# Kernel tuning notes

Hardware: AMD Instinct MI355X
Metric: run time of the kernel (lower is better)

## Reference

```python
import jax, jax.numpy as jnp
import numpy as np

EMBED = 1024
HEADS = 16


def setup_inputs() -> dict:
    key = jax.random.key(0)
    k1, k2, k3 = jax.random.split(key, 3)
    B, S, D = 2, 2048, EMBED
    x = jax.random.normal(k1, (B, S, D), dtype=jnp.float32)
    # nn.Linear weights: stored as [out, in]; y = x @ W.T
    w_qkv = jax.random.normal(k2, (3 * D, D), dtype=jnp.float32) * (D ** -0.5)
    w_out = jax.random.normal(k3, (D, D), dtype=jnp.float32) * (D ** -0.5)
    return {"x": x, "w_qkv": w_qkv, "w_out": w_out}


def reference(x, w_qkv, w_out):
    B, S, D = x.shape
    H = HEADS
    hd = D // H
    qkv = x @ w_qkv.T                       # [B, S, 3D]
    q, k, v = jnp.split(qkv, 3, axis=-1)
    # 'b l (head k) -> b head l k'
    def heads(t):
        return t.reshape(B, S, H, hd).transpose(0, 2, 1, 3)
    q, k, v = heads(q), heads(k), heads(v)
    scale = hd ** 0.5
    scores = jnp.einsum('bhqd,bhkd->bhqk', q, k) / scale
    probs = jax.nn.softmax(scores, axis=-1)
    out = jnp.einsum('bhqk,bhkd->bhqd', probs, v)  # [B, H, S, hd]
    out = out.transpose(0, 2, 1, 3).reshape(B, S, D)
    return out @ w_out.T
```

## Files before the change

kernel.cpp:

```cpp
#include <hip/hip_runtime.h>

typedef short short8 __attribute__((ext_vector_type(8)));
typedef short short4v __attribute__((ext_vector_type(4)));
typedef float floatx4 __attribute__((ext_vector_type(4)));
typedef unsigned short ushort_t;

#define EMBED 1024
#define HEADS 16
#define HD 64
#define SEQ 2048
#define BATCH 2
#define QSCALE 0.18033688f

__device__ inline ushort_t f2bf(float f) {
    unsigned int u = __float_as_uint(f);
    u += 0x7fff + ((u >> 16) & 1);
    return (ushort_t)(u >> 16);
}

typedef const __attribute__((address_space(1))) unsigned int* gas_t;
typedef __attribute__((address_space(3))) unsigned int* las_t;
__device__ inline void async_copy16(const ushort_t* g, ushort_t* l) {
    __builtin_amdgcn_global_load_lds((gas_t)g, (las_t)l, 16, 0, 0);
}

__global__ void cast3_kernel(const float* __restrict__ a, ushort_t* __restrict__ oa, int na,
                             const float* __restrict__ b, ushort_t* __restrict__ ob, int nb,
                             const float* __restrict__ c, ushort_t* __restrict__ oc, int nc) {
    int idx = (blockIdx.x * blockDim.x + threadIdx.x) * 4;
    const float* in; ushort_t* out;
    if (idx < na)            { in = a;  out = oa; }
    else if (idx < na + nb)  { in = b;  out = ob; idx -= na; }
    else if (idx < na + nb + nc) { in = c; out = oc; idx -= na + nb; }
    else return;
    float4 f = *(const float4*)(in + idx);
    ushort4 o;
    o.x = f2bf(f.x); o.y = f2bf(f.y); o.z = f2bf(f.z); o.w = f2bf(f.w);
    *(ushort4*)(out + idx) = o;
}

#define BM 128
#define BN 128
#define BK 64

template<int MODE>
__launch_bounds__(256, 3)
__global__ void gemm_bt(const ushort_t* __restrict__ A, const ushort_t* __restrict__ B,
                        float* __restrict__ outF,
                        ushort_t* __restrict__ qb, ushort_t* __restrict__ kb,
                        ushort_t* __restrict__ vtb,
                        int M, int N, int K) {
    __shared__ ushort_t As[BM * BK];
    __shared__ ushort_t Bs[BN * BK];
    const int id   = blockIdx.x;
    const int jj   = id >> 3;
    const int bm   = (id & 7) * 4 + (jj & 3);
    const int bn   = jj >> 2;
    const int t    = threadIdx.x;
    const int lane = t & 63;
    const int wave = t >> 6;
    const int wm   = (wave >> 1) * 64;
    const int wn   = (wave & 1) * 64;
    const int m0   = bm * BM;
    const int n0   = bn * BN;
    const int col  = lane & 15;
    const int quad = lane >> 4;

    const int srow = lane >> 3;
    const int sgr  = (lane & 7) ^ (srow & 7);
    const int slot0 = quad ^ (col & 7);

    floatx4 acc[4][4] = {};

    for (int k0 = 0; k0 < K; k0 += BK) {
        for (int half = 0; half < 4; ++half) {
            int row0 = wave * 32 + half * 8;
            int r = row0 + srow;
            async_copy16(A + (size_t)(m0 + r) * K + k0 + sgr * 8, &As[row0 * BK]);
            async_copy16(B + (size_t)(n0 + r) * K + k0 + sgr * 8, &Bs[row0 * BK]);
        }
        __syncthreads();
        short8 a[2][4], b[2][4];
        for (int i = 0; i < 4; ++i) {
            int base = (wm + i * 16 + col) * BK;
            a[0][i] = *(const short8*)(&As[base + slot0 * 8]);
            a[1][i] = *(const short8*)(&As[base + (slot0 ^ 4) * 8]);
        }
        for (int j = 0; j < 4; ++j) {
            int base = (wn + j * 16 + col) * BK;
            b[0][j] = *(const short8*)(&Bs[base + slot0 * 8]);
            b[1][j] = *(const short8*)(&Bs[base + (slot0 ^ 4) * 8]);
        }
        for (int kk = 0; kk < 2; ++kk)
            for (int i = 0; i < 4; ++i)
                for (int j = 0; j < 4; ++j)
                    acc[i][j] = __builtin_amdgcn_mfma_f32_16x16x32_bf16(a[kk][i], b[kk][j], acc[i][j], 0, 0, 0);
        __syncthreads();
    }

    for (int i = 0; i < 4; ++i)
        for (int j = 0; j < 4; ++j) {
            int n = n0 + wn + j * 16 + col;
            int mb = m0 + wm + i * 16 + quad * 4;
            if (MODE == 1) {
                for (int r = 0; r < 4; ++r)
                    outF[(size_t)(mb + r) * N + n] = acc[i][j][r];
            } else {
                int part = n >> 10;
                int within = n & 1023;
                int h = within >> 6, d = within & 63;
                int bb = mb >> 11, s = mb & 2047;
                if (part == 2) {
                    short4v pv;
                    pv.x = (short)f2bf(acc[i][j][0]); pv.y = (short)f2bf(acc[i][j][1]);
                    pv.z = (short)f2bf(acc[i][j][2]); pv.w = (short)f2bf(acc[i][j][3]);
                    *(short4v*)(vtb + (((size_t)bb * HEADS + h) * HD + d) * SEQ + s) = pv;
                } else {
                    ushort_t* dst = (part == 0) ? qb : kb;
                    const float scl = (part == 0) ? QSCALE : 1.0f;
                    for (int r = 0; r < 4; ++r)
                        dst[(((size_t)bb * HEADS + h) * SEQ + s + r) * HD + d] = f2bf(acc[i][j][r] * scl);
                }
            }
        }
}

__launch_bounds__(512, 4)
__global__ void attn_kernel(const ushort_t* __restrict__ qb_, const ushort_t* __restrict__ kb,
                            const ushort_t* __restrict__ vtb, ushort_t* __restrict__ attn) {
    __shared__ __align__(16) ushort_t lds[36864];
    const int id   = blockIdx.x;
    const int jj   = id >> 3;
    const int bh   = (id & 7) * 4 + (jj >> 4);
    const int qblk = jj & 15;
    const int t    = threadIdx.x;
    const int lane = t & 63;
    const int wave = t >> 6;
    const int g    = wave >> 2;
    const int wv   = wave & 3;
    const int col  = lane & 15;
    const int quad = lane >> 4;
    const int q0   = qblk * 128 + wv * 32;
    const int sw   = col & 7;
    const int srow = lane >> 3;
    const int sgr  = lane & 7;

    const ushort_t* Q  = qb_ + (size_t)bh * SEQ * HD;
    const ushort_t* Kp = kb  + (size_t)bh * SEQ * HD;
    const ushort_t* Vt = vtb + (size_t)bh * HD * SEQ;

    ushort_t* Kb0 = &lds[(g * 2) * 4096];
    ushort_t* Vb0 = &lds[16384 + (g * 2) * 4096];
    ushort_t* Pb  = &lds[32768 + wave * 512];

    auto stage = [&](int c, int buf) {
        int kt = c << 6;
        #pragma unroll
        for (int inst = 0; inst < 2; ++inst) {
            int row0 = wv * 16 + inst * 8;
            int r = row0 + srow;
            async_copy16(Kp + (size_t)(kt + r) * HD + (sgr ^ (r & 7)) * 8,
                         Kb0 + buf * 4096 + row0 * 64);
            async_copy16(Vt + (size_t)r * SEQ + kt + (sgr ^ (r & 7)) * 8,
                         Vb0 + buf * 4096 + row0 * 64);
        }
    };

    short8 qf[2][2];
    #pragma unroll
    for (int qt = 0; qt < 2; ++qt) {
        qf[qt][0] = *(const short8*)(Q + (size_t)(q0 + qt * 16 + col) * HD + quad * 8);
        qf[qt][1] = *(const short8*)(Q + (size_t)(q0 + qt * 16 + col) * HD + 32 + quad * 8);
    }

    floatx4 acc[2][4] = {};
    float lsum[2] = {0.f, 0.f};

    stage(g, 0);
    __syncthreads();

    for (int i = 0; i < 16; ++i) {
        const int cur = i & 1;
        if (i < 15) stage(2 * (i + 1) + g, cur ^ 1);
        const ushort_t* Kc = Kb0 + cur * 4096;
        const ushort_t* Vc = Vb0 + cur * 4096;

        #pragma unroll
        for (int h = 0; h < 2; ++h) {
            short8 kf[2][2], vf[4];
            #pragma unroll
            for (int nl = 0; nl < 2; ++nl) {
                int row = (2 * h + nl) * 16 + col;
                kf[nl][0] = *(const short8*)(Kc + row * 64 + ((quad ^ sw) * 8));
                kf[nl][1] = *(const short8*)(Kc + row * 64 + (((4 + quad) ^ sw) * 8));
            }
            #pragma unroll
            for (int d = 0; d < 4; ++d) {
                int row = d * 16 + col;
                vf[d] = *(const short8*)(Vc + row * 64 + (((4 * h + quad) ^ sw) * 8));
            }
            #pragma unroll
            for (int qt = 0; qt < 2; ++qt) {
                #pragma unroll
                for (int nl = 0; nl < 2; ++nl) {
                    floatx4 z = {};
                    z = __builtin_amdgcn_mfma_f32_16x16x32_bf16(kf[nl][0], qf[qt][0], z, 0, 0, 0);
                    z = __builtin_amdgcn_mfma_f32_16x16x32_bf16(kf[nl][1], qf[qt][1], z, 0, 0, 0);
                    unsigned u0 = __float_as_uint(__builtin_amdgcn_exp2f(z[0]));
                    unsigned u1 = __float_as_uint(__builtin_amdgcn_exp2f(z[1]));
                    unsigned u2 = __float_as_uint(__builtin_amdgcn_exp2f(z[2]));
                    unsigned u3 = __float_as_uint(__builtin_amdgcn_exp2f(z[3]));
                    lsum[qt] += (__uint_as_float(u0 & 0xffff0000u) + __uint_as_float(u1 & 0xffff0000u))
                              + (__uint_as_float(u2 & 0xffff0000u) + __uint_as_float(u3 & 0xffff0000u));
                    uint2 pk;
                    pk.x = __builtin_amdgcn_perm(u1, u0, 0x07060302u);
                    pk.y = __builtin_amdgcn_perm(u3, u2, 0x07060302u);
                    int gl = nl * 2 + (quad >> 1);
                    *(uint2*)(&Pb[col * 32 + ((gl ^ (col & 3)) << 3) + ((quad & 1) << 2)]) = pk;
                }
                short8 pf = *(const short8*)(&Pb[col * 32 + ((quad ^ (col & 3)) << 3)]);
                #pragma unroll
                for (int d = 0; d < 4; ++d)
                    acc[qt][d] = __builtin_amdgcn_mfma_f32_16x16x32_bf16(pf, vf[d], acc[qt][d], 0, 0, 0);
            }
        }
        __syncthreads();
    }

    float* fs = (float*)lds;
    const int slot = (wave * 64 + lane) * 20;
    floatx4 accK[4];
    float lsK;
    if (g == 0) {
        #pragma unroll
        for (int d = 0; d < 4; ++d) { *(floatx4*)(&fs[slot + d * 4]) = acc[1][d]; accK[d] = acc[0][d]; }
        fs[slot + 16] = lsum[1]; lsK = lsum[0];
    } else {
        #pragma unroll
        for (int d = 0; d < 4; ++d) { *(floatx4*)(&fs[slot + d * 4]) = acc[0][d]; accK[d] = acc[1][d]; }
        fs[slot + 16] = lsum[0]; lsK = lsum[1];
    }
    __syncthreads();
    const int pslot = ((wave ^ 4) * 64 + lane) * 20;
    #pragma unroll
    for (int d = 0; d < 4; ++d)
        accK[d] += *(const floatx4*)(&fs[pslot + d * 4]);
    float s = lsK + fs[pslot + 16];
    s += __shfl_xor(s, 16);
    s += __shfl_xor(s, 32);
    float inv[4];
    #pragma unroll
    for (int r = 0; r < 4; ++r)
        inv[r] = 1.0f / __shfl(s, quad * 4 + r);

    int b = bh >> 4, hh = bh & 15;
    #pragma unroll
    for (int d = 0; d < 4; ++d)
        #pragma unroll
        for (int r = 0; r < 4; ++r) {
            int row = q0 + g * 16 + quad * 4 + r;
            int cc  = hh * HD + d * 16 + col;
            attn[((size_t)b * SEQ + row) * EMBED + cc] = f2bf(accK[d][r] * inv[r]);
        }
}

extern "C" void kernel_launch(void* const* d_in, const int* in_sizes, int n_in,
                              void* d_out, int out_size, void* d_ws, size_t ws_size,
                              hipStream_t stream) {
    const float* x     = (const float*)d_in[0];
    const float* w_qkv = (const float*)d_in[1];
    const float* w_out = (const float*)d_in[2];
    float* out = (float*)d_out;

    char* ws = (char*)d_ws;
    size_t off = 0;
    ushort_t* x_bf    = (ushort_t*)(ws + off); off += (size_t)BATCH * SEQ * EMBED * 2;
    ushort_t* wqkv_bf = (ushort_t*)(ws + off); off += (size_t)3 * EMBED * EMBED * 2;
    ushort_t* wout_bf = (ushort_t*)(ws + off); off += (size_t)EMBED * EMBED * 2;
    ushort_t* q_buf   = (ushort_t*)(ws + off); off += (size_t)BATCH * HEADS * SEQ * HD * 2;
    ushort_t* k_buf   = (ushort_t*)(ws + off); off += (size_t)BATCH * HEADS * SEQ * HD * 2;
    ushort_t* vt_buf  = (ushort_t*)(ws + off); off += (size_t)BATCH * HEADS * SEQ * HD * 2;
    ushort_t* attn_bf = (ushort_t*)(ws + off); off += (size_t)BATCH * SEQ * EMBED * 2;

    int n_x = BATCH * SEQ * EMBED, n_wq = 3 * EMBED * EMBED, n_wo = EMBED * EMBED;
    int n_all = n_x + n_wq + n_wo;
    cast3_kernel<<<n_all / 1024, 256, 0, stream>>>(x, x_bf, n_x, w_qkv, wqkv_bf, n_wq,
                                                   w_out, wout_bf, n_wo);

    gemm_bt<0><<<768, 256, 0, stream>>>(
        x_bf, wqkv_bf, nullptr, q_buf, k_buf, vt_buf, BATCH * SEQ, 3 * EMBED, EMBED);

    attn_kernel<<<512, 512, 0, stream>>>(q_buf, k_buf, vt_buf, attn_bf);

    gemm_bt<1><<<256, 256, 0, stream>>>(
        attn_bf, wout_bf, out, nullptr, nullptr, nullptr, BATCH * SEQ, EMBED, EMBED);
}
```

Measured before the change: 178.8 us.

## Feed exp scores straight into PV MFMA, removing LDS transpose of P

```diff
diff --git a/kernel.cpp b/kernel.cpp
--- a/kernel.cpp
+++ b/kernel.cpp
@@ -128,7 +128,7 @@
 __launch_bounds__(512, 4)
 __global__ void attn_kernel(const ushort_t* __restrict__ qb_, const ushort_t* __restrict__ kb,
                             const ushort_t* __restrict__ vtb, ushort_t* __restrict__ attn) {
-    __shared__ __align__(16) ushort_t lds[36864];
+    __shared__ __align__(16) ushort_t lds[32768];
     const int id   = blockIdx.x;
     const int jj   = id >> 3;
     const int bh   = (id & 7) * 4 + (jj >> 4);
@@ -149,9 +149,8 @@
     const ushort_t* Kp = kb  + (size_t)bh * SEQ * HD;
     const ushort_t* Vt = vtb + (size_t)bh * HD * SEQ;
 
-    ushort_t* Kb0 = &lds[(g * 2) * 4096];
-    ushort_t* Vb0 = &lds[16384 + (g * 2) * 4096];
-    ushort_t* Pb  = &lds[32768 + wave * 512];
+    ushort_t* Kb0 = &lds[g * 8192];
+    ushort_t* Vb0 = &lds[16384 + g * 8192];
 
     auto stage = [&](int c, int buf) {
         int kt = c << 6;
@@ -187,7 +186,8 @@
 
         #pragma unroll
         for (int h = 0; h < 2; ++h) {
-            short8 kf[2][2], vf[4];
+            short8 kf[2][2];
+            short4v vf[4][2];
             #pragma unroll
             for (int nl = 0; nl < 2; ++nl) {
                 int row = (2 * h + nl) * 16 + col;
@@ -195,12 +195,16 @@
                 kf[nl][1] = *(const short8*)(Kc + row * 64 + (((4 + quad) ^ sw) * 8));
             }
             #pragma unroll
-            for (int d = 0; d < 4; ++d) {
-                int row = d * 16 + col;
-                vf[d] = *(const short8*)(Vc + row * 64 + (((4 * h + quad) ^ sw) * 8));
-            }
+            for (int dt = 0; dt < 4; ++dt)
+                #pragma unroll
+                for (int kl = 0; kl < 2; ++kl) {
+                    int ks = h * 2 + kl;
+                    int row = dt * 16 + col;
+                    int slot = (ks * 2 + (quad >> 1)) ^ sw;
+                    vf[dt][kl] = *(const short4v*)(Vc + row * 64 + slot * 8 + (quad & 1) * 4);
+                }
             #pragma unroll
-            for (int qt = 0; qt < 2; ++qt) {
+            for (int qt = 0; qt < 2; ++qt)
                 #pragma unroll
                 for (int nl = 0; nl < 2; ++nl) {
                     floatx4 z = {};
@@ -215,14 +219,12 @@
                     uint2 pk;
                     pk.x = __builtin_amdgcn_perm(u1, u0, 0x07060302u);
                     pk.y = __builtin_amdgcn_perm(u3, u2, 0x07060302u);
-                    int gl = nl * 2 + (quad >> 1);
-                    *(uint2*)(&Pb[col * 32 + ((gl ^ (col & 3)) << 3) + ((quad & 1) << 2)]) = pk;
+                    short4v pb = *(short4v*)&pk;
+                    #pragma unroll
+                    for (int dt = 0; dt < 4; ++dt)
+                        acc[qt][dt] = __builtin_amdgcn_mfma_f32_16x16x16bf16_1k(
+                            vf[dt][nl], pb, acc[qt][dt], 0, 0, 0);
                 }
-                short8 pf = *(const short8*)(&Pb[col * 32 + ((quad ^ (col & 3)) << 3)]);
-                #pragma unroll
-                for (int d = 0; d < 4; ++d)
-                    acc[qt][d] = __builtin_amdgcn_mfma_f32_16x16x32_bf16(pf, vf[d], acc[qt][d], 0, 0, 0);
-            }
         }
         __syncthreads();
     }
@@ -248,20 +250,19 @@
     float s = lsK + fs[pslot + 16];
     s += __shfl_xor(s, 16);
     s += __shfl_xor(s, 32);
-    float inv[4];
+    float inv = 1.0f / s;
+
+    int b = bh >> 4, hh = bh & 15;
+    int row = q0 + g * 16 + col;
     #pragma unroll
-    for (int r = 0; r < 4; ++r)
-        inv[r] = 1.0f / __shfl(s, quad * 4 + r);
-
-    int b = bh >> 4, hh = bh & 15;
-    #pragma unroll
-    for (int d = 0; d < 4; ++d)
-        #pragma unroll
-        for (int r = 0; r < 4; ++r) {
-            int row = q0 + g * 16 + quad * 4 + r;
-            int cc  = hh * HD + d * 16 + col;
-            attn[((size_t)b * SEQ + row) * EMBED + cc] = f2bf(accK[d][r] * inv[r]);
-        }
+    for (int dt = 0; dt < 4; ++dt) {
+        short4v o;
+        o.x = (short)f2bf(accK[dt][0] * inv);
+        o.y = (short)f2bf(accK[dt][1] * inv);
+        o.z = (short)f2bf(accK[dt][2] * inv);
+        o.w = (short)f2bf(accK[dt][3] * inv);
+        *(short4v*)(attn + ((size_t)b * SEQ + row) * EMBED + hh * HD + dt * 16 + quad * 4) = o;
+    }
 }
 
 extern "C" void kernel_launch(void* const* d_in, const int* in_sizes, int n_in,
```

Result: no change. 181.3 us (+1.4%).
